# Kernel tuning notes

Measured on AMD Instinct MI355X. Metric: run time of the kernel, lower is better.

## Reference

```python
import jax, jax.numpy as jnp
import numpy as np

B, T, D, H = 8, 2048, 256, 4
HD = D // H                      # head dim = 64
SCALE = float(np.sqrt(HD))       # math.sqrt(hd)
EPS = 1e-5                       # nn.LayerNorm default
NEG = -1e9                       # stand-in for -inf; sparsemax output identical (0)


def setup_inputs() -> dict:
    key = jax.random.key(0)
    ks = jax.random.split(key, 8)
    x = jax.random.normal(ks[0], (B, T, D), dtype=jnp.float32)
    key_padding_mask = jax.random.bernoulli(ks[1], 0.15, (B, T))
    w = lambda k: jax.random.normal(k, (D, D), dtype=jnp.float32) * 0.02
    return {
        "x": x,
        "key_padding_mask": key_padding_mask,
        "Wq": w(ks[2]), "Wk": w(ks[3]), "Wv": w(ks[4]), "Wo": w(ks[5]),
        "gamma": jnp.ones((D,), jnp.float32),
        "beta": jnp.zeros((D,), jnp.float32),
    }


def sparsemax(z):
    # exact sort-based sparsemax over last axis (Martins & Astudillo 2016)
    n = z.shape[-1]
    zs = -jnp.sort(-z, axis=-1)                      # descending
    k = jnp.arange(1, n + 1, dtype=z.dtype)
    cum = jnp.cumsum(zs, axis=-1)
    support = (1.0 + k * zs) > cum                   # k in support
    ksel = jnp.sum(support, axis=-1, keepdims=True)  # support size >= 1
    cum_k = jnp.take_along_axis(cum, ksel - 1, axis=-1)
    tau = (cum_k - 1.0) / ksel.astype(z.dtype)
    return jnp.maximum(z - tau, 0.0)


def _split(y):  # (B,T,D) -> (B,H,T,hd)
    return y.reshape(B, T, H, HD).transpose(0, 2, 1, 3)


def reference(x, key_padding_mask, Wq, Wk, Wv, Wo, gamma, beta):
    Q = _split(x @ Wq.T)
    K = _split(x @ Wk.T)
    V = _split(x @ Wv.T)
    scores = jnp.einsum('bhqd,bhkd->bhqk', Q, K) / SCALE     # (B,H,T,T)
    scores = jnp.where(key_padding_mask[:, None, None, :], NEG, scores)
    A = sparsemax(scores)
    out = jnp.einsum('bhqk,bhkd->bhqd', A, V)                # (B,H,T,hd)
    out = out.transpose(0, 2, 1, 3).reshape(B, T, D)
    y = out @ Wo.T + x                                       # out-proj + residual
    mu = jnp.mean(y, axis=-1, keepdims=True)
    var = jnp.mean(jnp.square(y - mu), axis=-1, keepdims=True)
    return (y - mu) / jnp.sqrt(var + EPS) * gamma + beta
```

## Files before the change

### kernel.cpp

```cpp
#include <hip/hip_runtime.h>

typedef unsigned short ushort_t;
typedef unsigned char uchar_t;

using bf16x8 = __attribute__((ext_vector_type(8))) short;
using f32x4  = __attribute__((ext_vector_type(4))) float;
using h2     = __attribute__((ext_vector_type(2))) _Float16;
using h8     = __attribute__((ext_vector_type(8))) _Float16;
using hc2    = __attribute__((ext_vector_type(2))) __fp16;
using hc8    = __attribute__((ext_vector_type(8))) __fp16;

#define B_  8
#define T_  2048
#define D_  256
#define H_  4
#define HD_ 64
#define BH_ (B_*H_)
#define M_  (B_*T_)

#define NX_   ((size_t)M_*D_)
#define NW_   ((size_t)D_*D_)
#define NCONV (NX_ + 4*NW_)

__device__ __forceinline__ float bf2f(ushort_t u) {
    union { unsigned int i; float f; } v; v.i = ((unsigned int)u) << 16; return v.f;
}
__device__ __forceinline__ ushort_t f2bf(float f) {
    union { float f; unsigned int i; } v; v.f = f;
    unsigned int u = v.i;
    u += 0x7FFFu + ((u >> 16) & 1u);
    return (ushort_t)(u >> 16);
}
__device__ __forceinline__ h2 pkh(float lo, float hi) {
    union { hc2 a; h2 b; } u;
    u.a = __builtin_amdgcn_cvt_pkrtz(lo, hi);
    return u.b;
}
__device__ __forceinline__ float dot2(h2 a, h2 b, float c) {
    union { h2 h; hc2 c2; } ua, ub; ua.h = a; ub.h = b;
    return __builtin_amdgcn_fdot2(ua.c2, ub.c2, c, false);
}
__device__ __forceinline__ f32x4 mfma_f16(h8 a, h8 b, f32x4 c) {
    union { h8 h; hc8 c8; } ua, ub; ua.h = a; ub.h = b;
    return __builtin_amdgcn_mfma_f32_16x16x32_f16(ua.c8, ub.c8, c, 0, 0, 0);
}
__device__ __forceinline__ f32x4 mfma_bf16(bf16x8 a, bf16x8 b, f32x4 c) {
    return __builtin_amdgcn_mfma_f32_16x16x32_bf16(a, b, c, 0, 0, 0);
}
__device__ __forceinline__ int is_bf16_inputs(const void* gamma) {
    return ((const unsigned int*)gamma)[0] == 0x3F803F80u;
}
union h2u { unsigned int u; int i; h2 h; };
union hu1 { _Float16 h; ushort_t u; };

__global__ __launch_bounds__(256) void conv_mask_kernel(
        const void* __restrict__ x,
        const void* __restrict__ Wq, const void* __restrict__ Wk,
        const void* __restrict__ Wv, const void* __restrict__ Wo,
        const void* __restrict__ gamma, ushort_t* __restrict__ dst,
        const uchar_t* __restrict__ mraw, ushort_t* __restrict__ mout) {
    int isbf = is_bf16_inputs(gamma);
    int tid = threadIdx.x;

    if (blockIdx.x < 16) {
        __shared__ int f_or1, f_ornz, f_max, cls;
        if (tid == 0) { f_or1 = 0; f_ornz = 0; f_max = 0; }
        __syncthreads();
        int lor1 = 0, lornz = 0, lmax = 0;
        for (int i = tid * 16; i < tid * 16 + 16; ++i) {
            int v = mraw[i];
            lmax = max(lmax, v);
            if ((i & 3) == 1) lor1 |= v;
            if ((i & 3) != 0) lornz |= v;
        }
        atomicOr(&f_or1, lor1); atomicOr(&f_ornz, lornz); atomicMax(&f_max, lmax);
        __syncthreads();
        if (tid == 0) {
            int c;
            if (f_max == 0)      c = 0;
            else if (f_max <= 1) c = f_ornz ? 0 : 1;
            else                 c = f_or1 ? 2 : 3;
            cls = c;
        }
        __syncthreads();
        int c = cls;
        int base = blockIdx.x * 1024;
        for (int e = base + tid; e < base + 1024; e += 256) {
            int m;
            if (c == 0)      m = mraw[e] != 0;
            else if (c == 1) m = ((const int*)mraw)[e] != 0;
            else if (c == 2) m = ((const ushort_t*)mraw)[e] != 0;
            else             m = ((const float*)mraw)[e] != 0.0f;
            hu1 cv; cv.h = m ? (_Float16)(-30000.0f) : (_Float16)0.0f;
            mout[e] = cv.u;
        }
    }

    size_t e = ((size_t)blockIdx.x * 256 + tid) * 8;
    if (e >= NCONV) return;
    const void* src; size_t off;
    if (e < NX_) { src = x; off = e; }
    else {
        size_t r = e - NX_; int wsel = (int)(r >> 16);
        src = (wsel == 0) ? Wq : (wsel == 1) ? Wk : (wsel == 2) ? Wv : Wo;
        off = r & 65535;
    }
    if (isbf) {
        *(bf16x8*)(dst + e) = *(const bf16x8*)((const ushort_t*)src + off);
    } else {
        const float4* s = (const float4*)((const float*)src + off);
        float4 a = s[0], b = s[1];
        ushort_t o8[8] = { f2bf(a.x), f2bf(a.y), f2bf(a.z), f2bf(a.w),
                           f2bf(b.x), f2bf(b.y), f2bf(b.z), f2bf(b.w) };
        *(bf16x8*)(dst + e) = *(bf16x8*)o8;
    }
}

__global__ __launch_bounds__(256) void qkv_kernel(
        const ushort_t* __restrict__ x,
        const ushort_t* __restrict__ Wq, const ushort_t* __restrict__ Wk,
        const ushort_t* __restrict__ Wv,
        ushort_t* __restrict__ Qs, ushort_t* __restrict__ Ks, ushort_t* __restrict__ Vt) {
    __shared__ __align__(16) ushort_t vtile[10240];
    int mt = blockIdx.x, mat = blockIdx.y;
    int tid = threadIdx.x, w = tid >> 6, l = tid & 63, lr = l & 15, lg = l >> 4;
    const ushort_t* W = (mat == 0) ? Wq : ((mat == 1) ? Wk : Wv);
    const ushort_t* wbase = W + (size_t)(w * 64 + lr) * 256 + lg * 8;
    const ushort_t* xbase = x + (size_t)(mt * 32 + lr) * 256 + lg * 8;

    f32x4 acc[2][4] = {};
    for (int kk = 0; kk < 256; kk += 32) {
        bf16x8 bfr[4];
        #pragma unroll
        for (int ct = 0; ct < 4; ++ct)
            bfr[ct] = *(const bf16x8*)(wbase + (size_t)ct * 16 * 256 + kk);
        #pragma unroll
        for (int rt = 0; rt < 2; ++rt) {
            bf16x8 afr = *(const bf16x8*)(xbase + (size_t)rt * 16 * 256 + kk);
            #pragma unroll
            for (int ct = 0; ct < 4; ++ct)
                acc[rt][ct] = mfma_bf16(afr, bfr[ct], acc[rt][ct]);
        }
    }

    int b = mt >> 6, t0 = (mt * 32) & (T_ - 1);
    if (mat != 2) {
        float scale = (mat == 0) ? 0.125f : 1.0f;
        #pragma unroll
        for (int rt = 0; rt < 2; ++rt) {
            #pragma unroll
            for (int r = 0; r < 4; ++r) {
                int row = rt * 16 + lg * 4 + r;
                #pragma unroll
                for (int ct = 0; ct < 4; ++ct) {
                    int col = w * 64 + ct * 16 + lr;
                    hu1 cv; cv.h = (_Float16)(acc[rt][ct][r] * scale);
                    vtile[row * 264 + col] = cv.u;
                }
            }
        }
        __syncthreads();
        ushort_t* dstm = (mat == 0) ? Qs : Ks;
        #pragma unroll
        for (int k = 0; k < 4; ++k) {
            int idx = tid + k * 256;
            int row = idx >> 5, seg = idx & 31;
            uint4 v = *(const uint4*)&vtile[row * 264 + seg * 8];
            int head = seg >> 3, hd0 = (seg & 7) * 8;
            *(uint4*)(dstm + ((size_t)((b * H_ + head) * T_ + t0 + row)) * HD_ + hd0) = v;
        }
    } else {
        #pragma unroll
        for (int rt = 0; rt < 2; ++rt) {
            #pragma unroll
            for (int r = 0; r < 4; ++r) {
                int row = rt * 16 + lg * 4 + r;
                #pragma unroll
                for (int ct = 0; ct < 4; ++ct) {
                    int col = w * 64 + ct * 16 + lr;
                    hu1 cv; cv.h = (_Float16)acc[rt][ct][r];
                    vtile[col * 40 + row] = cv.u;
                }
            }
        }
        __syncthreads();
        #pragma unroll
        for (int k = 0; k < 4; ++k) {
            int idx = tid + k * 256;
            int d = idx >> 2, seg = idx & 3;
            uint4 v = *(const uint4*)&vtile[d * 40 + seg * 8];
            int head = d >> 6, hd = d & 63;
            *(uint4*)(Vt + ((size_t)((b * H_ + head) * HD_ + hd)) * T_ + t0 + seg * 8) = v;
        }
    }
}

__global__ __launch_bounds__(256, 2) void attn_kernel(
        const ushort_t* __restrict__ Qs, const ushort_t* __restrict__ Ks,
        const ushort_t* __restrict__ Vt, const ushort_t* __restrict__ biasbuf,
        ushort_t* __restrict__ attn_out) {
    __shared__ float red[512];
    __shared__ unsigned int obuf[2 * 4 * 16 * 33];
    int lin = blockIdx.y * (T_ / 32) + blockIdx.x;
    int work = (lin & 7) * 256 + (lin >> 3);
    int qt = work & 63, bh = work >> 6;
    int b = bh >> 2, h = bh & 3;
    int tid = threadIdx.x, w = tid >> 6, l = tid & 63, lr = l & 15, lg = l >> 4;

    const ushort_t* Qb = Qs + (size_t)bh * T_ * HD_;
    const ushort_t* Kb = Ks + (size_t)bh * T_ * HD_;
    const ushort_t* Vb = Vt + (size_t)bh * HD_ * T_;
    const ushort_t* brow = biasbuf + b * T_;

    const ushort_t* qrowA = Qb + (size_t)(qt * 32 + lr) * HD_ + lg * 8;
    h8 bqA0 = *(const h8*)(qrowA);
    h8 bqA1 = *(const h8*)(qrowA + 32);
    h8 bqB0 = *(const h8*)(qrowA + 16 * HD_);
    h8 bqB1 = *(const h8*)(qrowA + 16 * HD_ + 32);

    const int key_base = w * 512;
    const h2 hzero = { (_Float16)0.0f, (_Float16)0.0f };
    const h2 hone  = { (_Float16)1.0f, (_Float16)1.0f };
    const h2 hdlt  = { (_Float16)0.0078125f, (_Float16)0.0078125f };

    h2 scpA[64], scpB[64];
    h2 zmA = { (_Float16)(-30000.0f), (_Float16)(-30000.0f) };
    h2 zmB = zmA;
    const ushort_t* kp = Kb + (size_t)(key_base + lr) * HD_ + lg * 8;
    h8 ak0 = *(const h8*)(kp);
    h8 ak1 = *(const h8*)(kp + 32);
    #pragma unroll
    for (int i = 0; i < 32; ++i) {
        h8 nk0, nk1;
        if (i < 31) {
            const ushort_t* kn = kp + (size_t)(i + 1) * 16 * HD_;
            nk0 = *(const h8*)(kn);
            nk1 = *(const h8*)(kn + 32);
        }
        f32x4 cA = {}, cB = {};
        cA = mfma_f16(ak0, bqA0, cA);
        cB = mfma_f16(ak0, bqB0, cB);
        cA = mfma_f16(ak1, bqA1, cA);
        cB = mfma_f16(ak1, bqB1, cB);
        uint2 bm = *(const uint2*)(brow + key_base + i * 16 + lg * 4);
        h2u b01, b23; b01.u = bm.x; b23.u = bm.y;
        h2 pA0 = pkh(cA[0], cA[1]) + b01.h;
        h2 pA1 = pkh(cA[2], cA[3]) + b23.h;
        h2 pB0 = pkh(cB[0], cB[1]) + b01.h;
        h2 pB1 = pkh(cB[2], cB[3]) + b23.h;
        zmA = __builtin_elementwise_max(zmA, __builtin_elementwise_max(pA0, pA1));
        zmB = __builtin_elementwise_max(zmB, __builtin_elementwise_max(pB0, pB1));
        scpA[2 * i]     = pA0;
        scpA[2 * i + 1] = pA1;
        scpB[2 * i]     = pB0;
        scpB[2 * i + 1] = pB1;
        if (i < 31) { ak0 = nk0; ak1 = nk1; }
    }
    float zmaxA = fmaxf((float)zmA[0], (float)zmA[1]);
    float zmaxB = fmaxf((float)zmB[0], (float)zmB[1]);
    zmaxA = fmaxf(zmaxA, __shfl_xor(zmaxA, 16, 64));
    zmaxA = fmaxf(zmaxA, __shfl_xor(zmaxA, 32, 64));
    zmaxB = fmaxf(zmaxB, __shfl_xor(zmaxB, 16, 64));
    zmaxB = fmaxf(zmaxB, __shfl_xor(zmaxB, 32, 64));

    float zsA = -3e38f, zsB = -3e38f;
    #pragma unroll
    for (int j = 0; j < 8; ++j) {
        h2 pA = scpA[8 * j], pB = scpB[8 * j];
        zsA = fmaxf(zsA, fmaxf((float)pA[0], (float)pA[1]));
        zsB = fmaxf(zsB, fmaxf((float)pB[0], (float)pB[1]));
    }
    zsA = fmaxf(zsA, __shfl_xor(zsA, 16, 64));
    zsA = fmaxf(zsA, __shfl_xor(zsA, 32, 64));
    zsB = fmaxf(zsB, __shfl_xor(zsB, 16, 64));
    zsB = fmaxf(zsB, __shfl_xor(zsB, 32, 64));
    float twA = zsA - 1.0f, twB = zsB - 1.0f;
    #pragma unroll
    for (int it = 0; it < 6; ++it) {
        float thA = (float)(_Float16)twA, trA = twA - thA;
        float thB = (float)(_Float16)twB, trB = twB - thB;
        h2 t1A = pkh(thA, thA), t2A = pkh(trA, trA);
        h2 t1B = pkh(thB, thB), t2B = pkh(trB, trB);
        float SA = 0.0f, SmA = 0.0f, SB = 0.0f, SmB = 0.0f;
        #pragma unroll
        for (int j = 0; j < 8; ++j) {
            h2 dA = (scpA[8 * j] - t1A) - t2A;
            h2 dB = (scpB[8 * j] - t1B) - t2B;
            h2 mA = __builtin_elementwise_max(dA, hzero);
            h2 mB = __builtin_elementwise_max(dB, hzero);
            SA = dot2(mA, hone, SA);
            SB = dot2(mB, hone, SB);
            SmA = dot2(__builtin_elementwise_min(mA, hdlt), hone, SmA);
            SmB = dot2(__builtin_elementwise_min(mB, hdlt), hone, SmB);
        }
        SA += __shfl_xor(SA, 16, 64);  SA += __shfl_xor(SA, 32, 64);
        SB += __shfl_xor(SB, 16, 64);  SB += __shfl_xor(SB, 32, 64);
        SmA += __shfl_xor(SmA, 16, 64); SmA += __shfl_xor(SmA, 32, 64);
        SmB += __shfl_xor(SmB, 16, 64); SmB += __shfl_xor(SmB, 32, 64);
        float CA = fmaxf(SmA * 128.0f, 0.125f);
        float CB = fmaxf(SmB * 128.0f, 0.125f);
        twA += (SA - 0.03125f) / CA;
        twB += (SB - 0.03125f) / CB;
    }

    if (lg == 0) {
        red[w * 32 + lr * 2]       = twA;  red[w * 32 + lr * 2 + 1]       = zmaxA;
        red[128 + w * 32 + lr * 2] = twB;  red[128 + w * 32 + lr * 2 + 1] = zmaxB;
    }
    __syncthreads();
    float t4A = 0.25f * (red[lr * 2] + red[32 + lr * 2]
                       + red[64 + lr * 2] + red[96 + lr * 2]);
    float zbA = fmaxf(fmaxf(red[lr * 2 + 1], red[32 + lr * 2 + 1]),
                      fmaxf(red[64 + lr * 2 + 1], red[96 + lr * 2 + 1]));
    float t4B = 0.25f * (red[128 + lr * 2] + red[160 + lr * 2]
                       + red[192 + lr * 2] + red[224 + lr * 2]);
    float zbB = fmaxf(fmaxf(red[128 + lr * 2 + 1], red[160 + lr * 2 + 1]),
                      fmaxf(red[192 + lr * 2 + 1], red[224 + lr * 2 + 1]));
    float tauA = fminf(fmaxf(t4A, zbA - 1.0f), zbA - 0.01f);
    float tauB = fminf(fmaxf(t4B, zbB - 1.0f), zbB - 0.01f);

    int pp = 1;
    float tpA, tpB, SpA, SpB;
    bool done;
    {
        float thA = (float)(_Float16)tauA, trA = tauA - thA;
        float thB = (float)(_Float16)tauB, trB = tauB - thB;
        h2 t1A = pkh(thA, thA), t2A = pkh(trA, trA);
        h2 t1B = pkh(thB, thB), t2B = pkh(trB, trB);
        float SaA = 0.0f, SbA = 0.0f, CaA = 0.0f, CbA = 0.0f;
        float SaB = 0.0f, SbB = 0.0f, CaB = 0.0f, CbB = 0.0f;
        #pragma unroll
        for (int p2 = 0; p2 < 64; p2 += 2) {
            h2 mA0 = __builtin_elementwise_max((scpA[p2]     - t1A) - t2A, hzero);
            h2 mA1 = __builtin_elementwise_max((scpA[p2 + 1] - t1A) - t2A, hzero);
            h2 mB0 = __builtin_elementwise_max((scpB[p2]     - t1B) - t2B, hzero);
            h2 mB1 = __builtin_elementwise_max((scpB[p2 + 1] - t1B) - t2B, hzero);
            SaA = dot2(mA0, hone, SaA);
            SbA = dot2(mA1, hone, SbA);
            SaB = dot2(mB0, hone, SaB);
            SbB = dot2(mB1, hone, SbB);
            CaA = dot2(__builtin_elementwise_min(mA0, hdlt), hone, CaA);
            CbA = dot2(__builtin_elementwise_min(mA1, hdlt), hone, CbA);
            CaB = dot2(__builtin_elementwise_min(mB0, hdlt), hone, CaB);
            CbB = dot2(__builtin_elementwise_min(mB1, hdlt), hone, CbB);
        }
        float SA = SaA + SbA, SmA = CaA + CbA;
        float SB = SaB + SbB, SmB = CaB + CbB;
        SA += __shfl_xor(SA, 16, 64);   SA += __shfl_xor(SA, 32, 64);
        SB += __shfl_xor(SB, 16, 64);   SB += __shfl_xor(SB, 32, 64);
        SmA += __shfl_xor(SmA, 16, 64); SmA += __shfl_xor(SmA, 32, 64);
        SmB += __shfl_xor(SmB, 16, 64); SmB += __shfl_xor(SmB, 32, 64);
        float* rr = red + pp * 256;
        if (lg == 0) {
            float4 v4 = { SA, SmA, SB, SmB };
            *(float4*)&rr[w * 64 + lr * 4] = v4;
        }
        __syncthreads();
        float SAb = 0.0f, SmAb = 0.0f, SBb = 0.0f, SmBb = 0.0f;
        #pragma unroll
        for (int w2 = 0; w2 < 4; ++w2) {
            float4 v4 = *(const float4*)&rr[w2 * 64 + lr * 4];
            SAb += v4.x; SmAb += v4.y; SBb += v4.z; SmBb += v4.w;
        }
        float CA = fmaxf(SmAb * 128.0f, 1.0f);
        float CB = fmaxf(SmBb * 128.0f, 1.0f);
        float stepA = (SAb - 1.0f) / CA;
        float stepB = (SBb - 1.0f) / CB;
        tpA = tauA; SpA = SAb; tauA += stepA;
        tpB = tauB; SpB = SBb; tauB += stepB;
        pp ^= 1;
        done = __all(fmaxf(fabsf(stepA), fabsf(stepB)) < 2e-4f);
    }

    for (int it = 1; it < 6 && !done; ++it) {
        float thA = (float)(_Float16)tauA, trA = tauA - thA;
        float thB = (float)(_Float16)tauB, trB = tauB - thB;
        h2 t1A = pkh(thA, thA), t2A = pkh(trA, trA);
        h2 t1B = pkh(thB, thB), t2B = pkh(trB, trB);
        float SaA = 0.0f, SbA = 0.0f, SaB = 0.0f, SbB = 0.0f;
        #pragma unroll
        for (int p2 = 0; p2 < 64; p2 += 2) {
            h2 mA0 = __builtin_elementwise_max((scpA[p2]     - t1A) - t2A, hzero);
            h2 mA1 = __builtin_elementwise_max((scpA[p2 + 1] - t1A) - t2A, hzero);
            h2 mB0 = __builtin_elementwise_max((scpB[p2]     - t1B) - t2B, hzero);
            h2 mB1 = __builtin_elementwise_max((scpB[p2 + 1] - t1B) - t2B, hzero);
            SaA = dot2(mA0, hone, SaA);
            SbA = dot2(mA1, hone, SbA);
            SaB = dot2(mB0, hone, SaB);
            SbB = dot2(mB1, hone, SbB);
        }
        float SA = SaA + SbA, SB = SaB + SbB;
        SA += __shfl_xor(SA, 16, 64); SA += __shfl_xor(SA, 32, 64);
        SB += __shfl_xor(SB, 16, 64); SB += __shfl_xor(SB, 32, 64);
        float* rr = red + pp * 256;
        if (lg == 0) {
            float2 v2 = { SA, SB };
            *(float2*)&rr[w * 32 + lr * 2] = v2;
        }
        __syncthreads();
        float SAb = 0.0f, SBb = 0.0f;
        #pragma unroll
        for (int w2 = 0; w2 < 4; ++w2) {
            float2 v2 = *(const float2*)&rr[w2 * 32 + lr * 2];
            SAb += v2.x; SBb += v2.y;
        }
        float dA = tauA - tpA, dB = tauB - tpB;
        float CA = (fabsf(dA) > 1e-7f)
                 ? fminf(fmaxf((SpA - SAb) / dA, 1.0f), 1e7f) : 1e7f;
        float CB = (fabsf(dB) > 1e-7f)
                 ? fminf(fmaxf((SpB - SBb) / dB, 1.0f), 1e7f) : 1e7f;
        float stepA = (SAb - 1.0f) / CA;
        float stepB = (SBb - 1.0f) / CB;
        tpA = tauA; SpA = SAb; tauA += stepA;
        tpB = tauB; SpB = SBb; tauB += stepB;
        pp ^= 1;
        done = __all(fmaxf(fabsf(stepA), fabsf(stepB)) < 2e-4f);
    }

    float thA = (float)(_Float16)tauA, trA = tauA - thA;
    float thB = (float)(_Float16)tauB, trB = tauB - thB;
    h2 t1A = pkh(thA, thA), t2A = pkh(trA, trA);
    h2 t1B = pkh(thB, thB), t2B = pkh(trB, trB);
    int idxA = 4 * (lr + 32 * (lg & 1));
    int idxB = idxA + 64;
    bool hi2 = (lg >> 1) != 0;
    f32x4 accA0 = {}, accA1 = {}, accA2 = {}, accA3 = {};
    f32x4 accB0 = {}, accB1 = {}, accB2 = {}, accB3 = {};
    const ushort_t* vb2 = Vb + (size_t)lr * T_ + key_base + lg * 8;
    h8 va0 = *(const h8*)(vb2);
    h8 va1 = *(const h8*)(vb2 + (size_t)16 * T_);
    h8 va2 = *(const h8*)(vb2 + (size_t)32 * T_);
    h8 va3 = *(const h8*)(vb2 + (size_t)48 * T_);
    #pragma unroll
    for (int c = 0; c < 16; ++c) {
        h8 na0, na1, na2, na3;
        if (c < 15) {
            const ushort_t* vp = vb2 + (c + 1) * 32;
            na0 = *(const h8*)(vp);
            na1 = *(const h8*)(vp + (size_t)16 * T_);
            na2 = *(const h8*)(vp + (size_t)32 * T_);
            na3 = *(const h8*)(vp + (size_t)48 * T_);
        }
        h2u pA0, pA1, pA2, pA3, pB0, pB1, pB2, pB3;
        pA0.h = __builtin_elementwise_max((scpA[4*c]   - t1A) - t2A, hzero);
        pA1.h = __builtin_elementwise_max((scpA[4*c+1] - t1A) - t2A, hzero);
        pA2.h = __builtin_elementwise_max((scpA[4*c+2] - t1A) - t2A, hzero);
        pA3.h = __builtin_elementwise_max((scpA[4*c+3] - t1A) - t2A, hzero);
        pB0.h = __builtin_elementwise_max((scpB[4*c]   - t1B) - t2B, hzero);
        pB1.h = __builtin_elementwise_max((scpB[4*c+1] - t1B) - t2B, hzero);
        pB2.h = __builtin_elementwise_max((scpB[4*c+2] - t1B) - t2B, hzero);
        pB3.h = __builtin_elementwise_max((scpB[4*c+3] - t1B) - t2B, hzero);
        int wAA0  = __builtin_amdgcn_ds_bpermute(idxA, pA0.i);
        int wAA0o = __builtin_amdgcn_ds_bpermute(idxA, pA2.i);
        int wAA1  = __builtin_amdgcn_ds_bpermute(idxA, pA1.i);
        int wAA1o = __builtin_amdgcn_ds_bpermute(idxA, pA3.i);
        int wAB0  = __builtin_amdgcn_ds_bpermute(idxB, pA0.i);
        int wAB0o = __builtin_amdgcn_ds_bpermute(idxB, pA2.i);
        int wAB1  = __builtin_amdgcn_ds_bpermute(idxB, pA1.i);
        int wAB1o = __builtin_amdgcn_ds_bpermute(idxB, pA3.i);
        int wBA0  = __builtin_amdgcn_ds_bpermute(idxA, pB0.i);
        int wBA0o = __builtin_amdgcn_ds_bpermute(idxA, pB2.i);
        int wBA1  = __builtin_amdgcn_ds_bpermute(idxA, pB1.i);
        int wBA1o = __builtin_amdgcn_ds_bpermute(idxA, pB3.i);
        int wBB0  = __builtin_amdgcn_ds_bpermute(idxB, pB0.i);
        int wBB0o = __builtin_amdgcn_ds_bpermute(idxB, pB2.i);
        int wBB1  = __builtin_amdgcn_ds_bpermute(idxB, pB1.i);
        int wBB1o = __builtin_amdgcn_ds_bpermute(idxB, pB3.i);
        union { int u[4]; h8 v8; } bbA, bbB;
        bbA.u[0] = hi2 ? wAA0o : wAA0;
        bbA.u[1] = hi2 ? wAA1o : wAA1;
        bbA.u[2] = hi2 ? wAB0o : wAB0;
        bbA.u[3] = hi2 ? wAB1o : wAB1;
        bbB.u[0] = hi2 ? wBA0o : wBA0;
        bbB.u[1] = hi2 ? wBA1o : wBA1;
        bbB.u[2] = hi2 ? wBB0o : wBB0;
        bbB.u[3] = hi2 ? wBB1o : wBB1;
        accA0 = mfma_f16(va0, bbA.v8, accA0);
        accB0 = mfma_f16(va0, bbB.v8, accB0);
        accA1 = mfma_f16(va1, bbA.v8, accA1);
        accB1 = mfma_f16(va1, bbB.v8, accB1);
        accA2 = mfma_f16(va2, bbA.v8, accA2);
        accB2 = mfma_f16(va2, bbB.v8, accB2);
        accA3 = mfma_f16(va3, bbA.v8, accA3);
        accB3 = mfma_f16(va3, bbB.v8, accB3);
        if (c < 15) { va0 = na0; va1 = na1; va2 = na2; va3 = na3; }
    }

    {
        int ob = w * 528 + lr * 33;
        h2u e0, e1, e2, e3, e4, e5, e6, e7;
        e0.h = pkh(accA0[0], accA0[1]); e1.h = pkh(accA0[2], accA0[3]);
        e2.h = pkh(accA1[0], accA1[1]); e3.h = pkh(accA1[2], accA1[3]);
        e4.h = pkh(accA2[0], accA2[1]); e5.h = pkh(accA2[2], accA2[3]);
        e6.h = pkh(accA3[0], accA3[1]); e7.h = pkh(accA3[2], accA3[3]);
        obuf[ob + 2 * lg]          = e0.u;
        obuf[ob + 2 * lg + 1]      = e1.u;
        obuf[ob + 8 + 2 * lg]      = e2.u;
        obuf[ob + 8 + 2 * lg + 1]  = e3.u;
        obuf[ob + 16 + 2 * lg]     = e4.u;
        obuf[ob + 16 + 2 * lg + 1] = e5.u;
        obuf[ob + 24 + 2 * lg]     = e6.u;
        obuf[ob + 24 + 2 * lg + 1] = e7.u;
        int ob2 = 2112 + ob;
        e0.h = pkh(accB0[0], accB0[1]); e1.h = pkh(accB0[2], accB0[3]);
        e2.h = pkh(accB1[0], accB1[1]); e3.h = pkh(accB1[2], accB1[3]);
        e4.h = pkh(accB2[0], accB2[1]); e5.h = pkh(accB2[2], accB2[3]);
        e6.h = pkh(accB3[0], accB3[1]); e7.h = pkh(accB3[2], accB3[3]);
        obuf[ob2 + 2 * lg]          = e0.u;
        obuf[ob2 + 2 * lg + 1]      = e1.u;
        obuf[ob2 + 8 + 2 * lg]      = e2.u;
        obuf[ob2 + 8 + 2 * lg + 1]  = e3.u;
        obuf[ob2 + 16 + 2 * lg]     = e4.u;
        obuf[ob2 + 16 + 2 * lg + 1] = e5.u;
        obuf[ob2 + 24 + 2 * lg]     = e6.u;
        obuf[ob2 + 24 + 2 * lg + 1] = e7.u;
    }
    __syncthreads();
    int hd = tid & 63;
    #pragma unroll
    for (int k = 0; k < 4; ++k) {
        int row = (tid >> 6) * 4 + k;
        float vA = 0.0f, vB = 0.0f;
        #pragma unroll
        for (int w2 = 0; w2 < 4; ++w2) {
            h2u pA; pA.u = obuf[w2 * 528 + row * 33 + (hd >> 1)];
            h2u pB; pB.u = obuf[2112 + w2 * 528 + row * 33 + (hd >> 1)];
            vA += (float)pA.h[hd & 1];
            vB += (float)pB.h[hd & 1];
        }
        int tgA = qt * 32 + row;
        int tgB = tgA + 16;
        attn_out[((size_t)(b * T_ + tgA)) * D_ + h * HD_ + hd] = f2bf(vA);
        attn_out[((size_t)(b * T_ + tgB)) * D_ + h * HD_ + hd] = f2bf(vB);
    }
}

__global__ __launch_bounds__(256, 2) void oproj_ln_kernel(
        const ushort_t* __restrict__ ao, const ushort_t* __restrict__ Wo,
        const void* __restrict__ xres, const void* __restrict__ gamma,
        const void* __restrict__ beta, void* __restrict__ out) {
    __shared__ float psum[4][32][2];
    int isbf = is_bf16_inputs(gamma);
    int mt = blockIdx.x;
    int tid = threadIdx.x, w = tid >> 6, l = tid & 63, lr = l & 15, lg = l >> 4;
    const ushort_t* abase = ao + (size_t)(mt * 32 + lr) * 256 + lg * 8;
    const ushort_t* wbase = Wo + (size_t)(w * 64 + lr) * 256 + lg * 8;

    f32x4 acc[2][4] = {};
    for (int kk = 0; kk < 256; kk += 32) {
        bf16x8 bfr[4];
        #pragma unroll
        for (int ct = 0; ct < 4; ++ct)
            bfr[ct] = *(const bf16x8*)(wbase + (size_t)ct * 16 * 256 + kk);
        #pragma unroll
        for (int rt = 0; rt < 2; ++rt) {
            bf16x8 afr = *(const bf16x8*)(abase + (size_t)rt * 16 * 256 + kk);
            #pragma unroll
            for (int ct = 0; ct < 4; ++ct)
                acc[rt][ct] = mfma_bf16(afr, bfr[ct], acc[rt][ct]);
        }
    }

    #pragma unroll
    for (int rt = 0; rt < 2; ++rt) {
        #pragma unroll
        for (int r = 0; r < 4; ++r) {
            int row = rt * 16 + lg * 4 + r;
            size_t gro = (size_t)(mt * 32 + row) * 256;
            float s = 0.0f, s2 = 0.0f;
            #pragma unroll
            for (int ct = 0; ct < 4; ++ct) {
                int col = w * 64 + ct * 16 + lr;
                float xr = isbf ? bf2f(((const ushort_t*)xres)[gro + col])
                                : ((const float*)xres)[gro + col];
                float yv = acc[rt][ct][r] + xr;
                acc[rt][ct][r] = yv;
                s += yv; s2 += yv * yv;
            }
            #pragma unroll
            for (int o = 1; o < 16; o <<= 1) {
                s  += __shfl_xor(s, o, 64);
                s2 += __shfl_xor(s2, o, 64);
            }
            if (lr == 0) { psum[w][row][0] = s; psum[w][row][1] = s2; }
        }
    }
    __syncthreads();

    float gv[4], bv[4];
    #pragma unroll
    for (int ct = 0; ct < 4; ++ct) {
        int col = w * 64 + ct * 16 + lr;
        gv[ct] = isbf ? bf2f(((const ushort_t*)gamma)[col]) : ((const float*)gamma)[col];
        bv[ct] = isbf ? bf2f(((const ushort_t*)beta)[col])  : ((const float*)beta)[col];
    }
    #pragma unroll
    for (int rt = 0; rt < 2; ++rt) {
        #pragma unroll
        for (int r = 0; r < 4; ++r) {
            int row = rt * 16 + lg * 4 + r;
            float S  = psum[0][row][0] + psum[1][row][0]
                     + psum[2][row][0] + psum[3][row][0];
            float S2 = psum[0][row][1] + psum[1][row][1]
                     + psum[2][row][1] + psum[3][row][1];
            float mean = S * (1.0f / 256.0f);
            float var  = S2 * (1.0f / 256.0f) - mean * mean;
            float rstd = rsqrtf(var + 1e-5f);
            size_t gro = (size_t)(mt * 32 + row) * 256;
            #pragma unroll
            for (int ct = 0; ct < 4; ++ct) {
                int col = w * 64 + ct * 16 + lr;
                float o = (acc[rt][ct][r] - mean) * rstd * gv[ct] + bv[ct];
                if (isbf) ((ushort_t*)out)[gro + col] = f2bf(o);
                else      ((float*)out)[gro + col] = o;
            }
        }
    }
}

extern "C" void kernel_launch(void* const* d_in, const int* in_sizes, int n_in,
                              void* d_out, int out_size, void* d_ws, size_t ws_size,
                              hipStream_t stream) {
    const void*     x     = d_in[0];
    const uchar_t*  mraw  = (const uchar_t*)d_in[1];
    const void*     Wq    = d_in[2];
    const void*     Wk    = d_in[3];
    const void*     Wv    = d_in[4];
    const void*     Wo    = d_in[5];
    const void*     gamma = d_in[6];
    const void*     beta  = d_in[7];

    char* ws = (char*)d_ws;
    const size_t OFF_XB   = 0;
    const size_t OFF_WB   = 8388608;
    const size_t OFF_QS   = 9437184;
    const size_t OFF_KS   = OFF_QS + 8388608;
    const size_t OFF_VT   = OFF_KS + 8388608;
    const size_t OFF_MB   = OFF_VT + 8388608;
    if (ws_size < OFF_MB + 32768) return;

    ushort_t* xb   = (ushort_t*)(ws + OFF_XB);
    ushort_t* Wqb  = (ushort_t*)(ws + OFF_WB);
    ushort_t* Wkb  = Wqb + NW_;
    ushort_t* Wvb  = Wkb + NW_;
    ushort_t* Wob  = Wvb + NW_;
    ushort_t* Qs   = (ushort_t*)(ws + OFF_QS);
    ushort_t* Ks   = (ushort_t*)(ws + OFF_KS);
    ushort_t* Vt   = (ushort_t*)(ws + OFF_VT);
    ushort_t* ao   = (ushort_t*)(ws + OFF_XB);
    ushort_t* mbuf = (ushort_t*)(ws + OFF_MB);

    conv_mask_kernel<<<(int)(NCONV / 8 / 256), 256, 0, stream>>>(
        x, Wq, Wk, Wv, Wo, gamma, xb, mraw, mbuf);
    qkv_kernel<<<dim3(M_ / 32, 3), 256, 0, stream>>>(xb, Wqb, Wkb, Wvb, Qs, Ks, Vt);
    attn_kernel<<<dim3(T_ / 32, BH_), 256, 0, stream>>>(Qs, Ks, Vt, mbuf, ao);
    oproj_ln_kernel<<<M_ / 32, 256, 0, stream>>>(ao, Wob, x, gamma, beta, d_out);
}
```

Measured before the change: 295.0 us.

## Deepen K/V register prefetch to two stages and skip redundant bf16 x copy

The attention kernel's K and V fragment loads now use a two-deep ring buffer in registers, prefetching two iterations ahead instead of one. This gives global load latency more time to hide behind the MFMA work. Separately, when inputs are already bf16, the conversion kernel no longer copies x and the QKV kernel reads the original x directly. This saves one pass over the activation tensor, at the cost of more live registers in attention.

```diff
diff --git a/kernel.cpp b/kernel.cpp
--- a/kernel.cpp
+++ b/kernel.cpp
@@ -98,6 +98,7 @@
 
     size_t e = ((size_t)blockIdx.x * 256 + tid) * 8;
     if (e >= NCONV) return;
+    if (isbf && e < NX_) return;
     const void* src; size_t off;
     if (e < NX_) { src = x; off = e; }
     else {
@@ -117,16 +118,18 @@
 }
 
 __global__ __launch_bounds__(256) void qkv_kernel(
-        const ushort_t* __restrict__ x,
+        const ushort_t* __restrict__ xb, const void* __restrict__ xorig,
+        const void* __restrict__ gamma,
         const ushort_t* __restrict__ Wq, const ushort_t* __restrict__ Wk,
         const ushort_t* __restrict__ Wv,
         ushort_t* __restrict__ Qs, ushort_t* __restrict__ Ks, ushort_t* __restrict__ Vt) {
     __shared__ __align__(16) ushort_t vtile[10240];
     int mt = blockIdx.x, mat = blockIdx.y;
     int tid = threadIdx.x, w = tid >> 6, l = tid & 63, lr = l & 15, lg = l >> 4;
+    const ushort_t* xs = is_bf16_inputs(gamma) ? (const ushort_t*)xorig : xb;
     const ushort_t* W = (mat == 0) ? Wq : ((mat == 1) ? Wk : Wv);
     const ushort_t* wbase = W + (size_t)(w * 64 + lr) * 256 + lg * 8;
-    const ushort_t* xbase = x + (size_t)(mt * 32 + lr) * 256 + lg * 8;
+    const ushort_t* xbase = xs + (size_t)(mt * 32 + lr) * 256 + lg * 8;
 
     f32x4 acc[2][4] = {};
     for (int kk = 0; kk < 256; kk += 32) {
@@ -227,21 +230,24 @@
     h2 zmA = { (_Float16)(-30000.0f), (_Float16)(-30000.0f) };
     h2 zmB = zmA;
     const ushort_t* kp = Kb + (size_t)(key_base + lr) * HD_ + lg * 8;
-    h8 ak0 = *(const h8*)(kp);
-    h8 ak1 = *(const h8*)(kp + 32);
+    h8 kb0[2], kb1[2];
+    kb0[0] = *(const h8*)(kp);
+    kb1[0] = *(const h8*)(kp + 32);
+    kb0[1] = *(const h8*)(kp + (size_t)16 * HD_);
+    kb1[1] = *(const h8*)(kp + (size_t)16 * HD_ + 32);
     #pragma unroll
     for (int i = 0; i < 32; ++i) {
-        h8 nk0, nk1;
-        if (i < 31) {
-            const ushort_t* kn = kp + (size_t)(i + 1) * 16 * HD_;
-            nk0 = *(const h8*)(kn);
-            nk1 = *(const h8*)(kn + 32);
+        h8 a0 = kb0[i & 1], a1 = kb1[i & 1];
+        if (i < 30) {
+            const ushort_t* kn = kp + (size_t)(i + 2) * 16 * HD_;
+            kb0[i & 1] = *(const h8*)(kn);
+            kb1[i & 1] = *(const h8*)(kn + 32);
         }
         f32x4 cA = {}, cB = {};
-        cA = mfma_f16(ak0, bqA0, cA);
-        cB = mfma_f16(ak0, bqB0, cB);
-        cA = mfma_f16(ak1, bqA1, cA);
-        cB = mfma_f16(ak1, bqB1, cB);
+        cA = mfma_f16(a0, bqA0, cA);
+        cB = mfma_f16(a0, bqB0, cB);
+        cA = mfma_f16(a1, bqA1, cA);
+        cB = mfma_f16(a1, bqB1, cB);
         uint2 bm = *(const uint2*)(brow + key_base + i * 16 + lg * 4);
         h2u b01, b23; b01.u = bm.x; b23.u = bm.y;
         h2 pA0 = pkh(cA[0], cA[1]) + b01.h;
@@ -254,7 +260,6 @@
         scpA[2 * i + 1] = pA1;
         scpB[2 * i]     = pB0;
         scpB[2 * i + 1] = pB1;
-        if (i < 31) { ak0 = nk0; ak1 = nk1; }
     }
     float zmaxA = fmaxf((float)zmA[0], (float)zmA[1]);
     float zmaxB = fmaxf((float)zmB[0], (float)zmB[1]);
@@ -427,19 +432,24 @@
     f32x4 accA0 = {}, accA1 = {}, accA2 = {}, accA3 = {};
     f32x4 accB0 = {}, accB1 = {}, accB2 = {}, accB3 = {};
     const ushort_t* vb2 = Vb + (size_t)lr * T_ + key_base + lg * 8;
-    h8 va0 = *(const h8*)(vb2);
-    h8 va1 = *(const h8*)(vb2 + (size_t)16 * T_);
-    h8 va2 = *(const h8*)(vb2 + (size_t)32 * T_);
-    h8 va3 = *(const h8*)(vb2 + (size_t)48 * T_);
+    h8 va[2][4];
+    #pragma unroll
+    for (int s = 0; s < 2; ++s) {
+        const ushort_t* vp = vb2 + s * 32;
+        va[s][0] = *(const h8*)(vp);
+        va[s][1] = *(const h8*)(vp + (size_t)16 * T_);
+        va[s][2] = *(const h8*)(vp + (size_t)32 * T_);
+        va[s][3] = *(const h8*)(vp + (size_t)48 * T_);
+    }
     #pragma unroll
     for (int c = 0; c < 16; ++c) {
-        h8 na0, na1, na2, na3;
-        if (c < 15) {
-            const ushort_t* vp = vb2 + (c + 1) * 32;
-            na0 = *(const h8*)(vp);
-            na1 = *(const h8*)(vp + (size_t)16 * T_);
-            na2 = *(const h8*)(vp + (size_t)32 * T_);
-            na3 = *(const h8*)(vp + (size_t)48 * T_);
+        h8 v0 = va[c & 1][0], v1 = va[c & 1][1], v2 = va[c & 1][2], v3 = va[c & 1][3];
+        if (c < 14) {
+            const ushort_t* vp = vb2 + (c + 2) * 32;
+            va[c & 1][0] = *(const h8*)(vp);
+            va[c & 1][1] = *(const h8*)(vp + (size_t)16 * T_);
+            va[c & 1][2] = *(const h8*)(vp + (size_t)32 * T_);
+            va[c & 1][3] = *(const h8*)(vp + (size_t)48 * T_);
         }
         h2u pA0, pA1, pA2, pA3, pB0, pB1, pB2, pB3;
         pA0.h = __builtin_elementwise_max((scpA[4*c]   - t1A) - t2A, hzero);
@@ -475,15 +485,14 @@
         bbB.u[1] = hi2 ? wBA1o : wBA1;
         bbB.u[2] = hi2 ? wBB0o : wBB0;
         bbB.u[3] = hi2 ? wBB1o : wBB1;
-        accA0 = mfma_f16(va0, bbA.v8, accA0);
-        accB0 = mfma_f16(va0, bbB.v8, accB0);
-        accA1 = mfma_f16(va1, bbA.v8, accA1);
-        accB1 = mfma_f16(va1, bbB.v8, accB1);
-        accA2 = mfma_f16(va2, bbA.v8, accA2);
-        accB2 = mfma_f16(va2, bbB.v8, accB2);
-        accA3 = mfma_f16(va3, bbA.v8, accA3);
-        accB3 = mfma_f16(va3, bbB.v8, accB3);
-        if (c < 15) { va0 = na0; va1 = na1; va2 = na2; va3 = na3; }
+        accA0 = mfma_f16(v0, bbA.v8, accA0);
+        accB0 = mfma_f16(v0, bbB.v8, accB0);
+        accA1 = mfma_f16(v1, bbA.v8, accA1);
+        accB1 = mfma_f16(v1, bbB.v8, accB1);
+        accA2 = mfma_f16(v2, bbA.v8, accA2);
+        accB2 = mfma_f16(v2, bbB.v8, accB2);
+        accA3 = mfma_f16(v3, bbA.v8, accA3);
+        accB3 = mfma_f16(v3, bbB.v8, accB3);
     }
 
     {
@@ -652,7 +661,8 @@
 
     conv_mask_kernel<<<(int)(NCONV / 8 / 256), 256, 0, stream>>>(
         x, Wq, Wk, Wv, Wo, gamma, xb, mraw, mbuf);
-    qkv_kernel<<<dim3(M_ / 32, 3), 256, 0, stream>>>(xb, Wqb, Wkb, Wvb, Qs, Ks, Vt);
+    qkv_kernel<<<dim3(M_ / 32, 3), 256, 0, stream>>>(
+        xb, x, gamma, Wqb, Wkb, Wvb, Qs, Ks, Vt);
     attn_kernel<<<dim3(T_ / 32, BH_), 256, 0, stream>>>(Qs, Ks, Vt, mbuf, ao);
     oproj_ln_kernel<<<M_ / 32, 256, 0, stream>>>(ao, Wob, x, gamma, beta, d_out);
 }
```

Result: no change. 293.2 us (median of 2 runs) (-0.6%).
